# Kernel tuning notes

Measured on AMD Instinct MI355X. Metric: run time of the kernel, lower is better.

The kernel has to match this reference:

```python
import jax, jax.numpy as jnp
import numpy as np

D, H, DK, DF = 512, 8, 64, 2048  # dim, heads, head_dim, forward_dim
EPS = 1e-5


def _layernorm(x, g, b):
    mu = jnp.mean(x, axis=-1, keepdims=True)
    var = jnp.mean(jnp.square(x - mu), axis=-1, keepdims=True)
    return (x - mu) * jax.lax.rsqrt(var + EPS) * g + b


def setup_inputs() -> dict:
    key = jax.random.key(0)
    ks = jax.random.split(key, 16)
    B, S = 2, 2048
    s_in = 1.0 / np.sqrt(D)
    s_ff = 1.0 / np.sqrt(DF)
    s_cat = 1.0 / np.sqrt(H * DK)
    return {
        "x": jax.random.normal(ks[0], (B, S, D), jnp.float32),
        # per-head Q/K/V projections stacked over heads: [H, D, DK]
        "Wq": jax.random.uniform(ks[1], (H, D, DK), jnp.float32, -s_in, s_in),
        "bq": jax.random.uniform(ks[2], (H, DK), jnp.float32, -s_in, s_in),
        "Wk": jax.random.uniform(ks[3], (H, D, DK), jnp.float32, -s_in, s_in),
        "bk": jax.random.uniform(ks[4], (H, DK), jnp.float32, -s_in, s_in),
        "Wv": jax.random.uniform(ks[5], (H, D, DK), jnp.float32, -s_in, s_in),
        "bv": jax.random.uniform(ks[6], (H, DK), jnp.float32, -s_in, s_in),
        "Wo": jax.random.uniform(ks[7], (H * DK, D), jnp.float32, -s_cat, s_cat),
        "bo": jax.random.uniform(ks[8], (D,), jnp.float32, -s_cat, s_cat),
        "ln1_g": jnp.ones((D,), jnp.float32),
        "ln1_b": jnp.zeros((D,), jnp.float32),
        "W1": jax.random.uniform(ks[9], (D, DF), jnp.float32, -s_in, s_in),
        "b1": jax.random.uniform(ks[10], (DF,), jnp.float32, -s_in, s_in),
        "W2": jax.random.uniform(ks[11], (DF, D), jnp.float32, -s_ff, s_ff),
        "b2": jax.random.uniform(ks[12], (D,), jnp.float32, -s_ff, s_ff),
        "ln2_g": jnp.ones((D,), jnp.float32),
        "ln2_b": jnp.zeros((D,), jnp.float32),
    }


def reference(x, Wq, bq, Wk, bk, Wv, bv, Wo, bo, ln1_g, ln1_b, W1, b1, W2, b2, ln2_g, ln2_b):
    # Per-head projections, batched over heads: [B,H,S,DK]
    q = jnp.einsum('bsd,hdk->bhsk', x, Wq) + bq[None, :, None, :]
    k = jnp.einsum('bsd,hdk->bhsk', x, Wk) + bk[None, :, None, :]
    v = jnp.einsum('bsd,hdk->bhsk', x, Wv) + bv[None, :, None, :]
    scale = 1.0 / np.sqrt(DK)
    scores = jnp.einsum('bhsk,bhtk->bhst', q, k) * scale  # [B,H,S,S]
    attn = jax.nn.softmax(scores, axis=-1)
    o = jnp.einsum('bhst,bhtk->bhsk', attn, v)  # [B,H,S,DK]
    # concat heads (head order matches torch cat over ModuleList)
    B, _, S, _ = o.shape
    o = o.transpose(0, 2, 1, 3).reshape(B, S, H * DK)
    attn_out = o @ Wo + bo
    # Residual 1 (dropout = identity in eval): LN(x + sublayer(x))
    h = _layernorm(x + attn_out, ln1_g, ln1_b)
    # FeedForward + Residual 2
    ff = jax.nn.relu(h @ W1 + b1) @ W2 + b2
    return _layernorm(h + ff, ln2_g, ln2_b)
```

## Files before the change

### kernel.cpp

```cpp
#include <hip/hip_runtime.h>


#define Dm   512
#define Hh   8
#define DKk  64
#define DFf  2048
#define Bb   2
#define Ss   2048
#define Nn   4096

typedef __attribute__((ext_vector_type(8))) short short8;
typedef __attribute__((ext_vector_type(4))) float f32x4;
typedef __attribute__((ext_vector_type(4))) short short4v;
typedef __attribute__((ext_vector_type(2))) int   int2v;

__device__ inline float bf2f(short s) {
    unsigned u = ((unsigned)(unsigned short)s) << 16;
    float f; __builtin_memcpy(&f, &u, 4); return f;
}
__device__ inline short f2bf(float f) {
    unsigned u; __builtin_memcpy(&u, &f, 4);
    u = (u + 0x7fff + ((u >> 16) & 1)) >> 16;
    return (short)u;
}
__device__ inline short cvt_elem(const void* p, long i, int f32flag) {
    if (f32flag) return f2bf(((const float*)p)[i]);
    return ((const short*)p)[i];
}
__device__ inline int detect_f32(const void* x) {
    const float* xf = (const float*)x;
    int ok = 0;
#pragma unroll
    for (int i = 0; i < 16; ++i) {
        float a = fabsf(xf[i]);
        ok += (a > 1e-8f && a < 1e4f) ? 1 : 0;
    }
    return ok >= 8;
}
__device__ inline void gload_lds16(const short* g, short* l) {
    __builtin_amdgcn_global_load_lds(
        (const __attribute__((address_space(1))) unsigned int*)g,
        (__attribute__((address_space(3))) unsigned int*)l, 16, 0, 0);
}

__global__ __launch_bounds__(256) void prep_kernel(
    const void* __restrict__ x, short* __restrict__ xb,
    const void* bq, const void* bk, const void* bv, const void* bo,
    const void* b1, const void* b2, const void* g1, const void* be1,
    const void* g2, const void* be2, short* __restrict__ smalls,
    const void* Wq, const void* Wk, const void* Wv,
    const void* Wo, const void* W1, const void* W2,
    short* __restrict__ WqkvT,
    short* __restrict__ WoT, short* __restrict__ W1T, short* __restrict__ W2T)
{
    const int f = detect_f32(x);
    int blk = blockIdx.x;
    if (blk < 512) {
        long base = (long)blk * 4096;
        for (int i = threadIdx.x; i < 4096; i += 256)
            xb[base + i] = cvt_elem(x, base + i, f);
        return;
    }
    if (blk == 512) {
        const void* srcs[10] = {bq, bk, bv, bo, b1, b2, g1, be1, g2, be2};
        const int   sz[10]   = {512, 512, 512, 512, 2048, 512, 512, 512, 512, 512};
        int off = 0;
        for (int j = 0; j < 10; ++j) {
            for (int i = threadIdx.x; i < sz[j]; i += 256)
                smalls[off + i] = cvt_elem(srcs[j], i, f);
            off += sz[j];
        }
        return;
    }
    __shared__ short tile[64][65];
    blk -= 513;
    const void* src; short* dst; long srcoff = 0; long dstoff = 0; int R, C, tr, tc;
    if (blk < 192) {
        int m = blk >> 6; int r = blk & 63; int h = r >> 3; int t = r & 7;
        src = (m == 0) ? Wq : (m == 1) ? Wk : Wv;
        dst = WqkvT + (long)m * 512 * 512;
        srcoff = (long)h * 512 * 64; dstoff = (long)h * 64 * 512;
        R = 512; C = 64; tr = t; tc = 0;
    } else if (blk < 256) {
        int r = blk - 192; src = Wo; dst = WoT; R = 512; C = 512; tr = r >> 3; tc = r & 7;
    } else if (blk < 512) {
        int r = blk - 256; src = W1; dst = W1T; R = 512; C = 2048; tr = r >> 5; tc = r & 31;
    } else {
        int r = blk - 512; src = W2; dst = W2T; R = 2048; C = 512; tr = r >> 3; tc = r & 7;
    }
    int r0 = tr * 64, c0 = tc * 64;
    for (int i = threadIdx.x; i < 4096; i += 256) {
        int rr = i >> 6, cc = i & 63;
        tile[rr][cc] = cvt_elem(src, srcoff + (long)(r0 + rr) * C + c0 + cc, f);
    }
    __syncthreads();
    for (int i = threadIdx.x; i < 4096; i += 256) {
        int cc = i >> 6, rr = i & 63;
        dst[dstoff + (long)(c0 + cc) * R + r0 + rr] = tile[rr][cc];
    }
}

#define MODE_F32       1
#define MODE_RELU_BF16 2
#define MODE_QKV       4

__global__ __launch_bounds__(256) void gemm_kernel(
    const short* __restrict__ A, const short* __restrict__ Bt,
    const short* __restrict__ bias, void* __restrict__ outp,
    void* __restrict__ out2, void* __restrict__ out3,
    int K, int Ncols, int mode, int Ktile)
{
    __shared__ short As[2][128 * 64];
    __shared__ short Bs[2][128 * 64];
    const int t    = threadIdx.x;
    const int lane = t & 63;
    const int wave = t >> 6;
    const int quad = lane >> 4;
    const int l15  = lane & 15;
    const int wm = wave >> 1, wn = wave & 1;
    const int row0 = blockIdx.x * 128;
    const int col0 = blockIdx.y * 128;
    const int kbase = blockIdx.z * Ktile;

    const int ri = lane >> 3;
    const int ct = (lane & 7) ^ ri;

    f32x4 acc[4][4];
#pragma unroll
    for (int i = 0; i < 4; ++i)
#pragma unroll
        for (int j = 0; j < 4; ++j) acc[i][j] = (f32x4){0.f, 0.f, 0.f, 0.f};

    auto stage = [&](int buf, int k0) {
#pragma unroll
        for (int p = 0; p < 4; ++p) {
            int r = wave * 32 + p * 8;
            gload_lds16(A + (long)(row0 + r + ri) * K + kbase + k0 + ct * 8,
                        &As[buf][r * 64 + lane * 8]);
        }
#pragma unroll
        for (int p = 0; p < 4; ++p) {
            int r = wave * 32 + p * 8;
            gload_lds16(Bt + (long)(col0 + r + ri) * K + kbase + k0 + ct * 8,
                        &Bs[buf][r * 64 + lane * 8]);
        }
    };

    stage(0, 0);
    int cur = 0;
    const int niter = Ktile >> 6;
    for (int it = 0; it < niter; ++it) {
        asm volatile("s_waitcnt vmcnt(0)" ::: "memory");
        __syncthreads();
        if (it + 1 < niter) stage(cur ^ 1, (it + 1) * 64);
#pragma unroll
        for (int kk = 0; kk < 2; ++kk) {
            short8 af[4], bfr[4];
#pragma unroll
            for (int mt = 0; mt < 4; ++mt) {
                int rowa = wm * 64 + mt * 16 + l15;
                af[mt] = *(const short8*)&As[cur][rowa * 64
                              + (((kk * 4 + quad) ^ (rowa & 7)) * 8)];
            }
#pragma unroll
            for (int nt = 0; nt < 4; ++nt) {
                int rowb = wn * 64 + nt * 16 + l15;
                bfr[nt] = *(const short8*)&Bs[cur][rowb * 64
                              + (((kk * 4 + quad) ^ (rowb & 7)) * 8)];
            }
#pragma unroll
            for (int mt = 0; mt < 4; ++mt)
#pragma unroll
                for (int nt = 0; nt < 4; ++nt)
                    acc[mt][nt] = __builtin_amdgcn_mfma_f32_16x16x32_bf16(
                        af[mt], bfr[nt], acc[mt][nt], 0, 0, 0);
        }
        cur ^= 1;
    }

    const int wrow0 = row0 + wm * 64;
    const int wcol0 = col0 + wn * 64;
    if (mode == MODE_QKV) {
        int m = wcol0 >> 9;
        if (m < 2) {
            short* out = (short*)(m == 0 ? outp : out2);
            float sc = (m == 0) ? 0.125f : 1.0f;
#pragma unroll
            for (int nt = 0; nt < 4; ++nt) {
                int col = wcol0 + nt * 16 + l15;
                float bb = bf2f(bias[col]);
                int cl = col & 511;
#pragma unroll
                for (int mt = 0; mt < 4; ++mt)
#pragma unroll
                    for (int r = 0; r < 4; ++r) {
                        int row = wrow0 + mt * 16 + quad * 4 + r;
                        out[(long)row * 512 + cl] = f2bf((acc[mt][nt][r] + bb) * sc);
                    }
            }
        } else {
            short* out = (short*)out3;
#pragma unroll
            for (int nt = 0; nt < 4; ++nt) {
                int col = wcol0 + nt * 16 + l15;
                float bb = bf2f(bias[col]);
                int cl = col - 1024;
                int h = cl >> 6, kk = cl & 63;
#pragma unroll
                for (int mt = 0; mt < 4; ++mt)
#pragma unroll
                    for (int r = 0; r < 4; ++r) {
                        int row = wrow0 + mt * 16 + quad * 4 + r;
                        int b = row >> 11, s = row & 2047;
                        out[((long)(b * Hh + h) * DKk + kk) * Ss + s] =
                            f2bf(acc[mt][nt][r] + bb);
                    }
            }
        }
    } else if (mode == MODE_F32) {
        float* out = (float*)outp + (long)blockIdx.z * Nn * Ncols;
        int zb = (blockIdx.z == 0);
#pragma unroll
        for (int nt = 0; nt < 4; ++nt) {
            int col = wcol0 + nt * 16 + l15;
            float bb = zb ? bf2f(bias[col]) : 0.f;
#pragma unroll
            for (int mt = 0; mt < 4; ++mt)
#pragma unroll
                for (int r = 0; r < 4; ++r) {
                    int row = wrow0 + mt * 16 + quad * 4 + r;
                    out[(long)row * Ncols + col] = acc[mt][nt][r] + bb;
                }
        }
    } else {
        short* out = (short*)outp;
#pragma unroll
        for (int nt = 0; nt < 4; ++nt) {
            int col = wcol0 + nt * 16 + l15;
            float bb = bf2f(bias[col]);
#pragma unroll
            for (int mt = 0; mt < 4; ++mt)
#pragma unroll
                for (int r = 0; r < 4; ++r) {
                    int row = wrow0 + mt * 16 + quad * 4 + r;
                    out[(long)row * Ncols + col] = f2bf(fmaxf(acc[mt][nt][r] + bb, 0.f));
                }
        }
    }
}

__global__ __launch_bounds__(256) void attn_kernel(
    const short* __restrict__ Q, const short* __restrict__ Kt,
    const short* __restrict__ Vt, short* __restrict__ po, float* __restrict__ ls)
{
    __shared__ __align__(16) short Ks[64 * 64];
    __shared__ __align__(16) short Vs[64 * 64];
    __shared__ __align__(16) short pbuf[4][32 * 72];
    const int lane = threadIdx.x & 63;
    const int wave = threadIdx.x >> 6;
    const int quad = lane >> 4;
    const int l15  = lane & 15;
    const int qt = blockIdx.x, bh = blockIdx.y, ks = blockIdx.z;
    const int b = bh >> 3, h = bh & 7;
    const int qrow = b * Ss + qt * 128 + wave * 32;

    short8 bq[2][2];
#pragma unroll
    for (int qh = 0; qh < 2; ++qh)
#pragma unroll
        for (int kk = 0; kk < 2; ++kk)
            bq[qh][kk] = *(const short8*)(Q + (long)(qrow + qh * 16 + l15) * Dm
                                          + h * DKk + kk * 32 + quad * 8);

    f32x4 o[2][4];
    float lsum[2] = {0.f, 0.f};
#pragma unroll
    for (int qh = 0; qh < 2; ++qh)
#pragma unroll
        for (int nt = 0; nt < 4; ++nt) o[qh][nt] = (f32x4){0.f, 0.f, 0.f, 0.f};

    const short* Kg = Kt + (long)b * Ss * Dm + h * DKk;
    const short* Vg = Vt + (long)bh * DKk * Ss;
    short* pbw = pbuf[wave];
    const int t00 = ks * 512;

    const int ri = lane >> 3;
    const int ct = (lane & 7) ^ ri;
    const int ldsrow0 = wave * 16;

    for (int it = 0; it < 8; ++it) {
        const int t0 = t00 + it * 64;
#pragma unroll
        for (int p = 0; p < 2; ++p) {
            int r = ldsrow0 + p * 8 + ri;
            gload_lds16(Kg + (long)(t0 + r) * Dm + ct * 8,
                        &Ks[(ldsrow0 + p * 8) * 64] + lane * 8);
        }
#pragma unroll
        for (int p = 0; p < 2; ++p) {
            int r = ldsrow0 + p * 8 + ri;
            gload_lds16(Vg + (long)r * Ss + t0 + ct * 8,
                        &Vs[(ldsrow0 + p * 8) * 64] + lane * 8);
        }
        asm volatile("s_waitcnt vmcnt(0)" ::: "memory");
        __syncthreads();

#pragma unroll
        for (int j = 0; j < 4; ++j) {
            short8 kf0 = *(const short8*)&Ks[(j * 16 + l15) * 64
                                             + ((quad ^ (l15 & 7)) * 8)];
            short8 kf1 = *(const short8*)&Ks[(j * 16 + l15) * 64
                                             + (((4 + quad) ^ (l15 & 7)) * 8)];
#pragma unroll
            for (int qh = 0; qh < 2; ++qh) {
                f32x4 sj = (f32x4){0.f, 0.f, 0.f, 0.f};
                sj = __builtin_amdgcn_mfma_f32_16x16x32_bf16(kf0, bq[qh][0], sj, 0, 0, 0);
                sj = __builtin_amdgcn_mfma_f32_16x16x32_bf16(kf1, bq[qh][1], sj, 0, 0, 0);
                int2v pk;
#pragma unroll
                for (int r2 = 0; r2 < 2; ++r2) {
                    float pa = __expf(fminf(sj[r2 * 2 + 0], 60.f));
                    float pc = __expf(fminf(sj[r2 * 2 + 1], 60.f));
                    lsum[qh] += pa + pc;
                    unsigned ua, uc;
                    __builtin_memcpy(&ua, &pa, 4);
                    __builtin_memcpy(&uc, &pc, 4);
                    pk[r2] = __builtin_amdgcn_perm(uc, ua, 0x07060302);
                }
                *(int2v*)&pbw[(qh * 16 + l15) * 72 + j * 16 + quad * 4] = pk;
            }
        }
        asm volatile("s_waitcnt lgkmcnt(0)" ::: "memory");
#pragma unroll
        for (int c = 0; c < 2; ++c) {
            short8 ap[2];
#pragma unroll
            for (int qh = 0; qh < 2; ++qh)
                ap[qh] = *(const short8*)&pbw[(qh * 16 + l15) * 72 + c * 32 + quad * 8];
#pragma unroll
            for (int nt = 0; nt < 4; ++nt) {
                short8 vf = *(const short8*)&Vs[(nt * 16 + l15) * 64
                                                + (((c * 4 + quad) ^ (l15 & 7)) * 8)];
#pragma unroll
                for (int qh = 0; qh < 2; ++qh)
                    o[qh][nt] = __builtin_amdgcn_mfma_f32_16x16x32_bf16(
                        ap[qh], vf, o[qh][nt], 0, 0, 0);
            }
        }
        asm volatile("" ::: "memory");
        __syncthreads();
    }

#pragma unroll
    for (int qh = 0; qh < 2; ++qh) {
        float v = lsum[qh];
        v += __shfl_xor(v, 16);
        v += __shfl_xor(v, 32);
        lsum[qh] = v;
    }
    short* pob = po + ((((long)bh * 16 + qt) * 4 + ks) * 128) * 64;
#pragma unroll
    for (int qh = 0; qh < 2; ++qh)
#pragma unroll
        for (int nt = 0; nt < 4; ++nt)
#pragma unroll
            for (int r = 0; r < 4; ++r)
                pob[(wave * 32 + qh * 16 + quad * 4 + r) * 64 + nt * 16 + l15] =
                    f2bf(o[qh][nt][r]);
    if (lane < 16) {
        long lbase = (((long)bh * 16 + qt) * 4 + ks) * 128 + wave * 32;
        ls[lbase + l15]      = lsum[0];
        ls[lbase + 16 + l15] = lsum[1];
    }
}

__global__ __launch_bounds__(256) void combine_kernel(
    const short* __restrict__ po, const float* __restrict__ ls,
    short* __restrict__ O)
{
    const int qt = blockIdx.x, bh = blockIdx.y;
    const int b = bh >> 3, h = bh & 7;
    const long base = ((long)bh * 16 + qt) * 4;
    const int tid = threadIdx.x;
    const int qloc = tid >> 4;
    const int dk0 = (tid & 15) * 4;
#pragma unroll
    for (int q0 = 0; q0 < 8; ++q0) {
        int q = q0 * 16 + qloc;
        f32x4 s = (f32x4){0.f, 0.f, 0.f, 0.f};
        float L = 0.f;
#pragma unroll
        for (int ksp = 0; ksp < 4; ++ksp) {
            short4v pv = *(const short4v*)(po + ((base + ksp) * 128 + q) * 64 + dk0);
#pragma unroll
            for (int i = 0; i < 4; ++i) s[i] += bf2f(pv[i]);
            L += ls[(base + ksp) * 128 + q];
        }
        float inv = 1.f / L;
        short4v ov;
#pragma unroll
        for (int i = 0; i < 4; ++i) ov[i] = f2bf(s[i] * inv);
        *(short4v*)(O + (long)(b * Ss + qt * 128 + q) * Dm + h * DKk + dk0) = ov;
    }
}

__global__ __launch_bounds__(256) void ln_kernel(
    const float* __restrict__ v0, const float* __restrict__ v1,
    const float* __restrict__ v2, const float* __restrict__ v3,
    const short* res,
    const short* __restrict__ g, const short* __restrict__ bt,
    void* out, const void* __restrict__ xdet)
{
    const int row = blockIdx.x, tid = threadIdx.x;
    const long base = (long)row * Dm;
    const long i0 = base + tid, i1 = base + 256 + tid;
    float x0 = v0[i0] + bf2f(res[i0]);
    float x1 = v0[i1] + bf2f(res[i1]);
    if (v1) { x0 += v1[i0]; x1 += v1[i1]; }
    if (v2) { x0 += v2[i0]; x1 += v2[i1]; }
    if (v3) { x0 += v3[i0]; x1 += v3[i1]; }

    __shared__ float red[8];
    const int wv = tid >> 6, ln = tid & 63;
    float s = x0 + x1;
#pragma unroll
    for (int mk = 1; mk < 64; mk <<= 1) s += __shfl_xor(s, mk);
    if (!ln) red[wv] = s;
    __syncthreads();
    float mean = (red[0] + red[1] + red[2] + red[3]) * (1.f / 512.f);
    float d0 = x0 - mean, d1 = x1 - mean;
    float q = d0 * d0 + d1 * d1;
#pragma unroll
    for (int mk = 1; mk < 64; mk <<= 1) q += __shfl_xor(q, mk);
    if (!ln) red[4 + wv] = q;
    __syncthreads();
    float rs = rsqrtf((red[4] + red[5] + red[6] + red[7]) * (1.f / 512.f) + 1e-5f);
    float y0 = d0 * rs * bf2f(g[tid])       + bf2f(bt[tid]);
    float y1 = d1 * rs * bf2f(g[256 + tid]) + bf2f(bt[256 + tid]);
    int f32out = xdet ? detect_f32(xdet) : 0;
    if (f32out) {
        float* o = (float*)out;
        o[i0] = y0; o[i1] = y1;
    } else {
        short* o = (short*)out;
        o[i0] = f2bf(y0); o[i1] = f2bf(y1);
    }
}

extern "C" void kernel_launch(void* const* d_in, const int* in_sizes, int n_in,
                              void* d_out, int out_size, void* d_ws, size_t ws_size,
                              hipStream_t stream)
{
    (void)in_sizes; (void)n_in; (void)out_size; (void)ws_size;
    const void* x   = d_in[0];
    const void* Wq  = d_in[1];  const void* bq  = d_in[2];
    const void* Wk  = d_in[3];  const void* bk  = d_in[4];
    const void* Wv  = d_in[5];  const void* bv  = d_in[6];
    const void* Wo  = d_in[7];  const void* bo  = d_in[8];
    const void* g1  = d_in[9];  const void* be1 = d_in[10];
    const void* W1  = d_in[11]; const void* b1  = d_in[12];
    const void* W2  = d_in[13]; const void* b2  = d_in[14];
    const void* g2  = d_in[15]; const void* be2 = d_in[16];

    char* ws = (char*)d_ws;
    size_t off = 0;
    auto alloc = [&](size_t bytes) -> void* {
        void* p = ws + off; off += (bytes + 255) & ~(size_t)255; return p;
    };
    short* WqkvT = (short*)alloc((size_t)3 * Dm * Dm * 2);
    short* WoT   = (short*)alloc((size_t)Dm * Dm * 2);
    short* W1T   = (short*)alloc((size_t)DFf * Dm * 2);
    short* W2T   = (short*)alloc((size_t)Dm * DFf * 2);
    short* xb    = (short*)alloc((size_t)Nn * Dm * 2);
    short* sm    = (short*)alloc((size_t)6656 * 2);
    char*  regA  = (char*)alloc((size_t)Nn * DFf * 2);
    short* Qb    = (short*)(regA);
    short* Kb    = (short*)(regA + (size_t)Nn * Dm * 2);
    short* Vt    = (short*)(regA + (size_t)Nn * Dm * 4);
    short* Ob    = (short*)(regA + (size_t)Nn * Dm * 6);
    short* u     = (short*)(regA);
    char*  regC  = (char*)alloc((size_t)4 * Nn * Dm * 4);
    short* po    = (short*)regC;
    float* wo_p  = (float*)regC;
    float* f2p   = (float*)regC;
    float* lsb   = (float*)alloc((size_t)16 * 16 * 4 * 128 * 4);
    short* h_bf  = xb;

    prep_kernel<<<1281, 256, 0, stream>>>(x, xb, bq, bk, bv, bo, b1, b2,
                                          g1, be1, g2, be2, sm,
                                          Wq, Wk, Wv, Wo, W1, W2,
                                          WqkvT, WoT, W1T, W2T);
    gemm_kernel<<<dim3(Nn / 128, 1536 / 128, 1), 256, 0, stream>>>(
        xb, WqkvT, sm + 0, Qb, Kb, Vt, Dm, 1536, MODE_QKV, Dm);
    attn_kernel<<<dim3(Ss / 128, Bb * Hh, 4), 256, 0, stream>>>(Qb, Kb, Vt, po, lsb);
    combine_kernel<<<dim3(Ss / 128, Bb * Hh), 256, 0, stream>>>(po, lsb, Ob);
    gemm_kernel<<<dim3(Nn / 128, Dm / 128, 2), 256, 0, stream>>>(
        Ob, WoT, sm + 1536, wo_p, nullptr, nullptr, Dm, Dm, MODE_F32, Dm / 2);
    ln_kernel<<<Nn, 256, 0, stream>>>(wo_p, wo_p + (long)Nn * Dm, nullptr, nullptr,
                                      xb, sm + 4608, sm + 5120, h_bf, nullptr);
    gemm_kernel<<<dim3(Nn / 128, DFf / 128, 1), 256, 0, stream>>>(
        h_bf, W1T, sm + 2048, u, nullptr, nullptr, Dm, DFf, MODE_RELU_BF16, Dm);
    gemm_kernel<<<dim3(Nn / 128, Dm / 128, 4), 256, 0, stream>>>(
        u, W2T, sm + 4096, f2p, nullptr, nullptr, DFf, Dm, MODE_F32, DFf / 4);
    ln_kernel<<<Nn, 256, 0, stream>>>(f2p, f2p + (long)Nn * Dm, f2p + (long)2 * Nn * Dm,
                                      f2p + (long)3 * Nn * Dm,
                                      h_bf, sm + 5632, sm + 6144, d_out, x);
}
```

Measured before the change: 209.5 us.

## Double-buffer attention K/V tiles, halve key splits, vectorize V store

The attention kernel now double-buffers its K and V LDS tiles, so the next tile's global-to-LDS load is issued while the current tile is computed, using a partial vmcnt wait and raw s_barrier. The key dimension is split two ways instead of four, which halves the partial outputs and the combine work but gives each block twice as many iterations and launches half as many blocks. The FFN2 GEMM split-K also drops from 4 to 2, cutting fp32 partial traffic into the final layernorm. The transposed V store in the QKV epilogue is vectorized to 4-element short stores. Fewer blocks may lower occupancy and parallelism on this GPU.

```diff
diff --git a/kernel.cpp b/kernel.cpp
--- a/kernel.cpp
+++ b/kernel.cpp
@@ -207,14 +207,14 @@
                 int cl = col - 1024;
                 int h = cl >> 6, kk = cl & 63;
 #pragma unroll
-                for (int mt = 0; mt < 4; ++mt)
-#pragma unroll
-                    for (int r = 0; r < 4; ++r) {
-                        int row = wrow0 + mt * 16 + quad * 4 + r;
-                        int b = row >> 11, s = row & 2047;
-                        out[((long)(b * Hh + h) * DKk + kk) * Ss + s] =
-                            f2bf(acc[mt][nt][r] + bb);
-                    }
+                for (int mt = 0; mt < 4; ++mt) {
+                    int row = wrow0 + mt * 16 + quad * 4;
+                    int b = row >> 11, s = row & 2047;
+                    short4v v4;
+#pragma unroll
+                    for (int r = 0; r < 4; ++r) v4[r] = f2bf(acc[mt][nt][r] + bb);
+                    *(short4v*)&out[((long)(b * Hh + h) * DKk + kk) * Ss + s] = v4;
+                }
             }
         }
     } else if (mode == MODE_F32) {
@@ -253,8 +253,8 @@
     const short* __restrict__ Q, const short* __restrict__ Kt,
     const short* __restrict__ Vt, short* __restrict__ po, float* __restrict__ ls)
 {
-    __shared__ __align__(16) short Ks[64 * 64];
-    __shared__ __align__(16) short Vs[64 * 64];
+    __shared__ __align__(16) short Ks[2][64 * 64];
+    __shared__ __align__(16) short Vs[2][64 * 64];
     __shared__ __align__(16) short pbuf[4][32 * 72];
     const int lane = threadIdx.x & 63;
     const int wave = threadIdx.x >> 6;
@@ -282,35 +282,45 @@
     const short* Kg = Kt + (long)b * Ss * Dm + h * DKk;
     const short* Vg = Vt + (long)bh * DKk * Ss;
     short* pbw = pbuf[wave];
-    const int t00 = ks * 512;
+    const int t00 = ks * 1024;
 
     const int ri = lane >> 3;
     const int ct = (lane & 7) ^ ri;
     const int ldsrow0 = wave * 16;
 
-    for (int it = 0; it < 8; ++it) {
-        const int t0 = t00 + it * 64;
+    auto stage = [&](int buf, int t0) {
 #pragma unroll
         for (int p = 0; p < 2; ++p) {
             int r = ldsrow0 + p * 8 + ri;
             gload_lds16(Kg + (long)(t0 + r) * Dm + ct * 8,
-                        &Ks[(ldsrow0 + p * 8) * 64] + lane * 8);
+                        &Ks[buf][(ldsrow0 + p * 8) * 64] + lane * 8);
         }
 #pragma unroll
         for (int p = 0; p < 2; ++p) {
             int r = ldsrow0 + p * 8 + ri;
             gload_lds16(Vg + (long)r * Ss + t0 + ct * 8,
-                        &Vs[(ldsrow0 + p * 8) * 64] + lane * 8);
-        }
-        asm volatile("s_waitcnt vmcnt(0)" ::: "memory");
-        __syncthreads();
+                        &Vs[buf][(ldsrow0 + p * 8) * 64] + lane * 8);
+        }
+    };
+
+    stage(0, t00);
+    for (int it = 0; it < 16; ++it) {
+        const int cur = it & 1;
+        if (it < 15) {
+            stage(cur ^ 1, t00 + (it + 1) * 64);
+            asm volatile("s_waitcnt vmcnt(4)" ::: "memory");
+        } else {
+            asm volatile("s_waitcnt vmcnt(0)" ::: "memory");
+        }
+        __builtin_amdgcn_s_barrier();
+        __builtin_amdgcn_sched_barrier(0);
 
 #pragma unroll
         for (int j = 0; j < 4; ++j) {
-            short8 kf0 = *(const short8*)&Ks[(j * 16 + l15) * 64
-                                             + ((quad ^ (l15 & 7)) * 8)];
-            short8 kf1 = *(const short8*)&Ks[(j * 16 + l15) * 64
-                                             + (((4 + quad) ^ (l15 & 7)) * 8)];
+            short8 kf0 = *(const short8*)&Ks[cur][(j * 16 + l15) * 64
+                                                  + ((quad ^ (l15 & 7)) * 8)];
+            short8 kf1 = *(const short8*)&Ks[cur][(j * 16 + l15) * 64
+                                                  + (((4 + quad) ^ (l15 & 7)) * 8)];
 #pragma unroll
             for (int qh = 0; qh < 2; ++qh) {
                 f32x4 sj = (f32x4){0.f, 0.f, 0.f, 0.f};
@@ -339,16 +349,17 @@
                 ap[qh] = *(const short8*)&pbw[(qh * 16 + l15) * 72 + c * 32 + quad * 8];
 #pragma unroll
             for (int nt = 0; nt < 4; ++nt) {
-                short8 vf = *(const short8*)&Vs[(nt * 16 + l15) * 64
-                                                + (((c * 4 + quad) ^ (l15 & 7)) * 8)];
+                short8 vf = *(const short8*)&Vs[cur][(nt * 16 + l15) * 64
+                                                     + (((c * 4 + quad) ^ (l15 & 7)) * 8)];
 #pragma unroll
                 for (int qh = 0; qh < 2; ++qh)
                     o[qh][nt] = __builtin_amdgcn_mfma_f32_16x16x32_bf16(
                         ap[qh], vf, o[qh][nt], 0, 0, 0);
             }
         }
-        asm volatile("" ::: "memory");
-        __syncthreads();
+        asm volatile("s_waitcnt lgkmcnt(0)" ::: "memory");
+        __builtin_amdgcn_s_barrier();
+        __builtin_amdgcn_sched_barrier(0);
     }
 
 #pragma unroll
@@ -358,7 +369,7 @@
         v += __shfl_xor(v, 32);
         lsum[qh] = v;
     }
-    short* pob = po + ((((long)bh * 16 + qt) * 4 + ks) * 128) * 64;
+    short* pob = po + ((((long)bh * 16 + qt) * 2 + ks) * 128) * 64;
 #pragma unroll
     for (int qh = 0; qh < 2; ++qh)
 #pragma unroll
@@ -368,7 +379,7 @@
                 pob[(wave * 32 + qh * 16 + quad * 4 + r) * 64 + nt * 16 + l15] =
                     f2bf(o[qh][nt][r]);
     if (lane < 16) {
-        long lbase = (((long)bh * 16 + qt) * 4 + ks) * 128 + wave * 32;
+        long lbase = (((long)bh * 16 + qt) * 2 + ks) * 128 + wave * 32;
         ls[lbase + l15]      = lsum[0];
         ls[lbase + 16 + l15] = lsum[1];
     }
@@ -380,7 +391,7 @@
 {
     const int qt = blockIdx.x, bh = blockIdx.y;
     const int b = bh >> 3, h = bh & 7;
-    const long base = ((long)bh * 16 + qt) * 4;
+    const long base = ((long)bh * 16 + qt) * 2;
     const int tid = threadIdx.x;
     const int qloc = tid >> 4;
     const int dk0 = (tid & 15) * 4;
@@ -390,7 +401,7 @@
         f32x4 s = (f32x4){0.f, 0.f, 0.f, 0.f};
         float L = 0.f;
 #pragma unroll
-        for (int ksp = 0; ksp < 4; ++ksp) {
+        for (int ksp = 0; ksp < 2; ++ksp) {
             short4v pv = *(const short4v*)(po + ((base + ksp) * 128 + q) * 64 + dk0);
 #pragma unroll
             for (int i = 0; i < 4; ++i) s[i] += bf2f(pv[i]);
@@ -479,11 +490,11 @@
     short* Vt    = (short*)(regA + (size_t)Nn * Dm * 4);
     short* Ob    = (short*)(regA + (size_t)Nn * Dm * 6);
     short* u     = (short*)(regA);
-    char*  regC  = (char*)alloc((size_t)4 * Nn * Dm * 4);
+    char*  regC  = (char*)alloc((size_t)2 * Nn * Dm * 4);
     short* po    = (short*)regC;
     float* wo_p  = (float*)regC;
     float* f2p   = (float*)regC;
-    float* lsb   = (float*)alloc((size_t)16 * 16 * 4 * 128 * 4);
+    float* lsb   = (float*)alloc((size_t)16 * 16 * 2 * 128 * 4);
     short* h_bf  = xb;
 
     prep_kernel<<<1281, 256, 0, stream>>>(x, xb, bq, bk, bv, bo, b1, b2,
@@ -492,7 +503,7 @@
                                           WqkvT, WoT, W1T, W2T);
     gemm_kernel<<<dim3(Nn / 128, 1536 / 128, 1), 256, 0, stream>>>(
         xb, WqkvT, sm + 0, Qb, Kb, Vt, Dm, 1536, MODE_QKV, Dm);
-    attn_kernel<<<dim3(Ss / 128, Bb * Hh, 4), 256, 0, stream>>>(Qb, Kb, Vt, po, lsb);
+    attn_kernel<<<dim3(Ss / 128, Bb * Hh, 2), 256, 0, stream>>>(Qb, Kb, Vt, po, lsb);
     combine_kernel<<<dim3(Ss / 128, Bb * Hh), 256, 0, stream>>>(po, lsb, Ob);
     gemm_kernel<<<dim3(Nn / 128, Dm / 128, 2), 256, 0, stream>>>(
         Ob, WoT, sm + 1536, wo_p, nullptr, nullptr, Dm, Dm, MODE_F32, Dm / 2);
@@ -500,9 +511,8 @@
                                       xb, sm + 4608, sm + 5120, h_bf, nullptr);
     gemm_kernel<<<dim3(Nn / 128, DFf / 128, 1), 256, 0, stream>>>(
         h_bf, W1T, sm + 2048, u, nullptr, nullptr, Dm, DFf, MODE_RELU_BF16, Dm);
-    gemm_kernel<<<dim3(Nn / 128, Dm / 128, 4), 256, 0, stream>>>(
-        u, W2T, sm + 4096, f2p, nullptr, nullptr, DFf, Dm, MODE_F32, DFf / 4);
-    ln_kernel<<<Nn, 256, 0, stream>>>(f2p, f2p + (long)Nn * Dm, f2p + (long)2 * Nn * Dm,
-                                      f2p + (long)3 * Nn * Dm,
+    gemm_kernel<<<dim3(Nn / 128, Dm / 128, 2), 256, 0, stream>>>(
+        u, W2T, sm + 4096, f2p, nullptr, nullptr, DFf, Dm, MODE_F32, DFf / 2);
+    ln_kernel<<<Nn, 256, 0, stream>>>(f2p, f2p + (long)Nn * Dm, nullptr, nullptr,
                                       h_bf, sm + 5632, sm + 6144, d_out, x);
 }
```

Result: slower. 216.8 us (+3.5%).

## Store split-K partials as bf16, use exp2 softmax, vectorize V-transpose stores

Applied to the files above, without the earlier changes.

The split-K GEMM partial outputs for the Wo and W2 projections are now stored as bf16 instead of fp32, and the LayerNorm kernels read bf16 partials. This halves the write and read traffic of the partial buffers. The attention softmax now uses the hardware exp2 with the log2(e) factor folded into the Q scale. The transposed V store in the QKV epilogue writes four bf16 values per store instead of scalar writes. Rounding each partial sum to bf16 before reduction adds accuracy loss.

```diff
diff --git a/kernel.cpp b/kernel.cpp
--- a/kernel.cpp
+++ b/kernel.cpp
@@ -100,9 +100,11 @@
     }
 }
 
-#define MODE_F32       1
+#define MODE_PART_BF16 1
 #define MODE_RELU_BF16 2
 #define MODE_QKV       4
+
+#define QSCALE 0.18033688011112042f
 
 __global__ __launch_bounds__(256) void gemm_kernel(
     const short* __restrict__ A, const short* __restrict__ Bt,
@@ -184,7 +186,7 @@
         int m = wcol0 >> 9;
         if (m < 2) {
             short* out = (short*)(m == 0 ? outp : out2);
-            float sc = (m == 0) ? 0.125f : 1.0f;
+            float sc = (m == 0) ? QSCALE : 1.0f;
 #pragma unroll
             for (int nt = 0; nt < 4; ++nt) {
                 int col = wcol0 + nt * 16 + l15;
@@ -207,18 +209,18 @@
                 int cl = col - 1024;
                 int h = cl >> 6, kk = cl & 63;
 #pragma unroll
-                for (int mt = 0; mt < 4; ++mt)
-#pragma unroll
-                    for (int r = 0; r < 4; ++r) {
-                        int row = wrow0 + mt * 16 + quad * 4 + r;
-                        int b = row >> 11, s = row & 2047;
-                        out[((long)(b * Hh + h) * DKk + kk) * Ss + s] =
-                            f2bf(acc[mt][nt][r] + bb);
-                    }
+                for (int mt = 0; mt < 4; ++mt) {
+                    int row = wrow0 + mt * 16 + quad * 4;
+                    int b = row >> 11, s = row & 2047;
+                    short4v v4;
+#pragma unroll
+                    for (int r = 0; r < 4; ++r) v4[r] = f2bf(acc[mt][nt][r] + bb);
+                    *(short4v*)&out[((long)(b * Hh + h) * DKk + kk) * Ss + s] = v4;
+                }
             }
         }
-    } else if (mode == MODE_F32) {
-        float* out = (float*)outp + (long)blockIdx.z * Nn * Ncols;
+    } else if (mode == MODE_PART_BF16) {
+        short* out = (short*)outp + (long)blockIdx.z * Nn * Ncols;
         int zb = (blockIdx.z == 0);
 #pragma unroll
         for (int nt = 0; nt < 4; ++nt) {
@@ -229,7 +231,7 @@
 #pragma unroll
                 for (int r = 0; r < 4; ++r) {
                     int row = wrow0 + mt * 16 + quad * 4 + r;
-                    out[(long)row * Ncols + col] = acc[mt][nt][r] + bb;
+                    out[(long)row * Ncols + col] = f2bf(acc[mt][nt][r] + bb);
                 }
         }
     } else {
@@ -319,8 +321,8 @@
                 int2v pk;
 #pragma unroll
                 for (int r2 = 0; r2 < 2; ++r2) {
-                    float pa = __expf(fminf(sj[r2 * 2 + 0], 60.f));
-                    float pc = __expf(fminf(sj[r2 * 2 + 1], 60.f));
+                    float pa = __builtin_amdgcn_exp2f(fminf(sj[r2 * 2 + 0], 86.f));
+                    float pc = __builtin_amdgcn_exp2f(fminf(sj[r2 * 2 + 1], 86.f));
                     lsum[qh] += pa + pc;
                     unsigned ua, uc;
                     __builtin_memcpy(&ua, &pa, 4);
@@ -405,8 +407,8 @@
 }
 
 __global__ __launch_bounds__(256) void ln_kernel(
-    const float* __restrict__ v0, const float* __restrict__ v1,
-    const float* __restrict__ v2, const float* __restrict__ v3,
+    const short* __restrict__ v0, const short* __restrict__ v1,
+    const short* __restrict__ v2, const short* __restrict__ v3,
     const short* res,
     const short* __restrict__ g, const short* __restrict__ bt,
     void* out, const void* __restrict__ xdet)
@@ -414,11 +416,11 @@
     const int row = blockIdx.x, tid = threadIdx.x;
     const long base = (long)row * Dm;
     const long i0 = base + tid, i1 = base + 256 + tid;
-    float x0 = v0[i0] + bf2f(res[i0]);
-    float x1 = v0[i1] + bf2f(res[i1]);
-    if (v1) { x0 += v1[i0]; x1 += v1[i1]; }
-    if (v2) { x0 += v2[i0]; x1 += v2[i1]; }
-    if (v3) { x0 += v3[i0]; x1 += v3[i1]; }
+    float x0 = bf2f(v0[i0]) + bf2f(res[i0]);
+    float x1 = bf2f(v0[i1]) + bf2f(res[i1]);
+    if (v1) { x0 += bf2f(v1[i0]); x1 += bf2f(v1[i1]); }
+    if (v2) { x0 += bf2f(v2[i0]); x1 += bf2f(v2[i1]); }
+    if (v3) { x0 += bf2f(v3[i0]); x1 += bf2f(v3[i1]); }
 
     __shared__ float red[8];
     const int wv = tid >> 6, ln = tid & 63;
@@ -479,10 +481,10 @@
     short* Vt    = (short*)(regA + (size_t)Nn * Dm * 4);
     short* Ob    = (short*)(regA + (size_t)Nn * Dm * 6);
     short* u     = (short*)(regA);
-    char*  regC  = (char*)alloc((size_t)4 * Nn * Dm * 4);
+    char*  regC  = (char*)alloc((size_t)4 * Nn * Dm * 2 * 2);
     short* po    = (short*)regC;
-    float* wo_p  = (float*)regC;
-    float* f2p   = (float*)regC;
+    short* wo_p  = (short*)regC;
+    short* f2p   = (short*)regC;
     float* lsb   = (float*)alloc((size_t)16 * 16 * 4 * 128 * 4);
     short* h_bf  = xb;
 
@@ -495,13 +497,13 @@
     attn_kernel<<<dim3(Ss / 128, Bb * Hh, 4), 256, 0, stream>>>(Qb, Kb, Vt, po, lsb);
     combine_kernel<<<dim3(Ss / 128, Bb * Hh), 256, 0, stream>>>(po, lsb, Ob);
     gemm_kernel<<<dim3(Nn / 128, Dm / 128, 2), 256, 0, stream>>>(
-        Ob, WoT, sm + 1536, wo_p, nullptr, nullptr, Dm, Dm, MODE_F32, Dm / 2);
+        Ob, WoT, sm + 1536, wo_p, nullptr, nullptr, Dm, Dm, MODE_PART_BF16, Dm / 2);
     ln_kernel<<<Nn, 256, 0, stream>>>(wo_p, wo_p + (long)Nn * Dm, nullptr, nullptr,
                                       xb, sm + 4608, sm + 5120, h_bf, nullptr);
     gemm_kernel<<<dim3(Nn / 128, DFf / 128, 1), 256, 0, stream>>>(
         h_bf, W1T, sm + 2048, u, nullptr, nullptr, Dm, DFf, MODE_RELU_BF16, Dm);
     gemm_kernel<<<dim3(Nn / 128, Dm / 128, 4), 256, 0, stream>>>(
-        u, W2T, sm + 4096, f2p, nullptr, nullptr, DFf, Dm, MODE_F32, DFf / 4);
+        u, W2T, sm + 4096, f2p, nullptr, nullptr, DFf, Dm, MODE_PART_BF16, DFf / 4);
     ln_kernel<<<Nn, 256, 0, stream>>>(f2p, f2p + (long)Nn * Dm, f2p + (long)2 * Nn * Dm,
                                       f2p + (long)3 * Nn * Dm,
                                       h_bf, sm + 5632, sm + 6144, d_out, x);
```

Result: faster. 202.1 us (-3.5%).
